# Optimization experiments

Measured on AMD Instinct MI355X. Metric: run time of the kernel, lower is better.

## Reference

```python
import jax, jax.numpy as jnp
import numpy as np
from jax.ops import segment_sum, segment_max

B, P, NP, EP = 128, 16, 256, 1280
EPG, ODIM, NH = 2048, 256, 128
EPS = 1e-5


def _bn(x, g, b):
    # BatchNorm1d (training-mode batch statistics), biased variance like torch
    mu = x.mean(0)
    var = ((x - mu) ** 2).mean(0)
    return g * (x - mu) * jax.lax.rsqrt(var + EPS) + b


def _gat(feat, src, dst, W, al, ar, resW, bias):
    # DGL GATConv: fc -> per-head attn logits -> leaky_relu -> edge softmax over dst -> aggregate; + residual fc + bias
    n = feat.shape[0]
    H, D = al.shape
    z = (feat @ W).reshape(n, H, D)
    el = (z * al).sum(-1)                                  # [n,H]
    er = (z * ar).sum(-1)
    e = jax.nn.leaky_relu(el[src] + er[dst], 0.2)          # [E,H]
    m = segment_max(e, dst, num_segments=n)
    ex = jnp.exp(e - m[dst])
    s = segment_sum(ex, dst, num_segments=n)
    a = ex / (s[dst] + 1e-9)
    rst = segment_sum(a[:, :, None] * z[src], dst, num_segments=n)  # [n,H,D]
    res = (feat @ resW).reshape(n, H, D)
    return (rst + res + bias.reshape(1, H, D)).reshape(n, H * D)


def _plane(feat, src, dst, p):
    # PlaneGraphEncoder forward (eval: dropout off)
    h = _gat(feat, src, dst, p['W1'], p['al1'], p['ar1'], p['res1'], p['b1'])
    h = jax.nn.relu(_bn(h, p['g1'], p['be1']))
    h = _gat(h, src, dst, p['W2'], p['al2'], p['ar2'], p['res2'], p['b2'])
    h = jax.nn.relu(_bn(h, p['g2'], p['be2']))
    rep = h.mean(0)                                        # dgl.mean_nodes -> [32]
    d = jax.nn.relu(_bn(h @ p['dW1'] + p['db1'], p['dg'], p['dbe']))
    recon = d @ p['dW2'] + p['db2']                        # [n,1]
    rloss = jnp.mean((recon - feat) ** 2)
    return rep, rloss


def _masked_gc(h, src, dst, mask_f, W, b):
    # DGL GraphConv(norm='both') with edge_weight = mask[src]*mask[dst]; structural degrees, clamp>=1
    n = h.shape[0]
    ones = jnp.ones(src.shape[0], h.dtype)
    d_out = jnp.maximum(segment_sum(ones, src, num_segments=n), 1.0)
    d_in = jnp.maximum(segment_sum(ones, dst, num_segments=n), 1.0)
    ew = mask_f[src] * mask_f[dst]                         # [E]
    hs = h * jax.lax.rsqrt(d_out)[:, None]
    agg = segment_sum(ew[:, None] * hs[src], dst, num_segments=n)
    return (agg * jax.lax.rsqrt(d_in)[:, None]) @ W + b


def _forward(plane_feat, original_features,
             W1, al1, ar1, res1, b1, g1, be1,
             W2, al2, ar2, res2, b2, g2, be2,
             dW1, db1, dg, dbe, dW2, db2,
             ft_W, ft_b, ft_g, ft_be, gc_W, gc_b, gbn_g, gbn_be,
             c1_W, c1_b, ln_g, ln_be, c2_W, c2_b,
             plane_src, plane_dst, patient_src, patient_dst, mask):
    pp = dict(W1=W1, al1=al1, ar1=ar1, res1=res1, b1=b1, g1=g1, be1=be1,
              W2=W2, al2=al2, ar2=ar2, res2=res2, b2=b2, g2=g2, be2=be2,
              dW1=dW1, db1=db1, dg=dg, dbe=dbe, dW2=dW2, db2=db2)
    enc_b = jax.vmap(_plane, in_axes=(0, 0, 0, None))      # over patients
    enc_pb = jax.vmap(enc_b, in_axes=(1, 1, 1, 0))         # over planes (params axis 0)
    reps, rlosses = enc_pb(plane_feat, plane_src, plane_dst, pp)   # [P,B,32], [P,B]
    plane_rep = jnp.transpose(reps, (1, 0, 2)).reshape(plane_feat.shape[0], -1)  # [B, P*32]
    avg_recon = rlosses.mean()                             # sum / (B*P)

    x = jnp.concatenate([original_features, plane_rep], axis=1)   # [B, fused]
    h = jax.nn.relu(_bn(x @ ft_W + ft_b, ft_g, ft_be))
    mask_f = mask.astype(h.dtype)
    h_sum = h
    for i in range(3):
        hn = _masked_gc(h, patient_src, patient_dst, mask_f, gc_W[i], gc_b[i])
        hn = jax.nn.relu(_bn(hn, gbn_g[i], gbn_be[i]))
        h = hn + h
        h_sum = h_sum + h
    h = h_sum / 4.0                                        # mean over [h0,h1,h2,h3]

    z = h @ c1_W + c1_b
    mu = z.mean(-1, keepdims=True)
    var = ((z - mu) ** 2).mean(-1, keepdims=True)
    z = jax.nn.relu(ln_g * (z - mu) * jax.lax.rsqrt(var + EPS) + ln_be)
    logits = z @ c2_W + c2_b
    return logits, avg_recon


def setup_inputs() -> dict:
    key = jax.random.key(0)
    ks = iter(jax.random.split(key, 64))
    f = lambda shape, s=0.1: jax.random.normal(next(ks), shape, jnp.float32) * s
    inp = dict(
        plane_feat=f((B, P, NP, 1), 1.0),
        plane_src=jax.random.randint(next(ks), (B, P, EP), 0, NP, jnp.int32),
        plane_dst=jax.random.randint(next(ks), (B, P, EP), 0, NP, jnp.int32),
        patient_src=jax.random.randint(next(ks), (EPG,), 0, B, jnp.int32),
        patient_dst=jax.random.randint(next(ks), (EPG,), 0, B, jnp.int32),
        original_features=f((B, ODIM), 1.0),
        mask=jax.random.randint(next(ks), (B,), 0, 2, jnp.int32),
        # per-plane encoder params, stacked over P
        W1=f((P, 1, 128)), al1=f((P, 2, 64)), ar1=f((P, 2, 64)),
        res1=f((P, 1, 128)), b1=f((P, 128)),
        g1=jnp.ones((P, 128)), be1=jnp.zeros((P, 128)),
        W2=f((P, 128, 32)), al2=f((P, 1, 32)), ar2=f((P, 1, 32)),
        res2=f((P, 128, 32)), b2=f((P, 32)),
        g2=jnp.ones((P, 32)), be2=jnp.zeros((P, 32)),
        dW1=f((P, 32, 128)), db1=f((P, 128)),
        dg=jnp.ones((P, 128)), dbe=jnp.zeros((P, 128)),
        dW2=f((P, 128, 1)), db2=f((P, 1)),
        # patient-level params
        ft_W=f((ODIM + P * 32, NH)), ft_b=f((NH,)),
        ft_g=jnp.ones((NH,)), ft_be=jnp.zeros((NH,)),
        gc_W=f((3, NH, NH)), gc_b=f((3, NH)),
        gbn_g=jnp.ones((3, NH)), gbn_be=jnp.zeros((3, NH)),
        c1_W=f((NH, NH // 2)), c1_b=f((NH // 2,)),
        ln_g=jnp.ones((NH // 2,)), ln_be=jnp.zeros((NH // 2,)),
        c2_W=f((NH // 2, 2)), c2_b=f((2,)),
    )
    return inp


def reference(plane_feat, plane_src, plane_dst, patient_src, patient_dst,
              original_features, mask,
              W1, al1, ar1, res1, b1, g1, be1,
              W2, al2, ar2, res2, b2, g2, be2,
              dW1, db1, dg, dbe, dW2, db2,
              ft_W, ft_b, ft_g, ft_be, gc_W, gc_b, gbn_g, gbn_be,
              c1_W, c1_b, ln_g, ln_be, c2_W, c2_b):
    return _forward(plane_feat, original_features,
                    W1, al1, ar1, res1, b1, g1, be1,
                    W2, al2, ar2, res2, b2, g2, be2,
                    dW1, db1, dg, dbe, dW2, db2,
                    ft_W, ft_b, ft_g, ft_be, gc_W, gc_b, gbn_g, gbn_be,
                    c1_W, c1_b, ln_g, ln_be, c2_W, c2_b,
                    plane_src, plane_dst, patient_src, patient_dst, mask)
```

## Files before the change

kernel.cpp:

```cpp
#include <hip/hip_runtime.h>

#define B_    128
#define P_    16
#define NP_   256
#define EP_   1280
#define EPG_  2048
#define ODIM_ 256
#define NH_   128

typedef __attribute__((ext_vector_type(8))) short s8_t;
typedef __attribute__((ext_vector_type(4))) short s4_t;
typedef __attribute__((ext_vector_type(4))) float f4_t;

__device__ __forceinline__ unsigned short f2b(float x) {
  unsigned u = __builtin_bit_cast(unsigned, x);
  u = (u + 0x7fffu + ((u >> 16) & 1u)) >> 16;
  return (unsigned short)u;
}
__device__ __forceinline__ float b2f(short x) {
  unsigned u = ((unsigned)(unsigned short)x) << 16;
  return __builtin_bit_cast(float, u);
}

struct SmemA {
  float f[256];
  union {
    __align__(16) unsigned short wT1[64 * 136];
    __align__(16) unsigned short z2[256 * 40];
  } u1;
  __align__(16) unsigned short dW1T[128 * 36];
  union {
    struct { float S0a[256]; float S1a[256]; } a;
    float redf[512];
  } u2;
  float el2[256], er2[256];
  union {
    struct { float abg0[128], abg1[128], abg2[128]; } a;
    struct { float al2v[32], ar2v[32], dW2v[128]; } b;
  } u3;
  union {
    int cnt[256];
    struct { float scA[32], shA[32], dscA[64], dshA[64]; } b;
  } u4;
  unsigned short esrc[1280];
  int wtot[4];
  float r8[4][8]; float stat[8]; float wA[2], wB[2];
  float rlacc;
};

__global__ __launch_bounds__(256, 3) void plane_enc(
    const float* __restrict__ feat, const int* __restrict__ esrcg, const int* __restrict__ edstg,
    const float* __restrict__ W1, const float* __restrict__ al1, const float* __restrict__ ar1,
    const float* __restrict__ res1, const float* __restrict__ b1, const float* __restrict__ g1,
    const float* __restrict__ be1,
    const float* __restrict__ W2, const float* __restrict__ al2, const float* __restrict__ ar2,
    const float* __restrict__ res2, const float* __restrict__ g2, const float* __restrict__ be2,
    const float* __restrict__ dW1, const float* __restrict__ dg, const float* __restrict__ dbe,
    const float* __restrict__ dW2, const float* __restrict__ db2,
    float* __restrict__ rep_out, float* __restrict__ rloss_out)
{
  __shared__ SmemA s;
  const int g = blockIdx.x;
  const int p = g & 15;
  const int t = threadIdx.x;
  const int lane = t & 63, wv = t >> 6;
  const int l15 = lane & 15, quad = lane >> 4;

  s.f[t] = feat[g * NP_ + t];
  if (t == 0) s.rlacc = 0.f;
  s.u4.cnt[t] = 0;
  __syncthreads();

  const int* gs = esrcg + g * EP_;
  const int* gd = edstg + g * EP_;
  for (int k = t; k < EP_; k += 256) atomicAdd(&s.u4.cnt[gd[k]], 1);
  __syncthreads();
  int v = s.u4.cnt[t];
  int incl = v;
  #pragma unroll
  for (int off = 1; off < 64; off <<= 1) {
    int n = __shfl_up(incl, off, 64);
    if (lane >= off) incl += n;
  }
  if (lane == 63) s.wtot[wv] = incl;
  __syncthreads();
  int woff = 0;
  for (int w = 0; w < wv; w++) woff += s.wtot[w];
  const int myStart = woff + incl - v;
  const int myDeg = v;
  __syncthreads();
  s.u4.cnt[t] = myStart;
  __syncthreads();
  for (int k = t; k < EP_; k += 256) {
    int d = gd[k];
    int pos = atomicAdd(&s.u4.cnt[d], 1);
    s.esrc[pos] = (unsigned short)gs[k];
  }
  {
    const float* W2g = W2 + p * 4096;
    const float* Rg  = res2 + p * 4096;
    for (int q = 0; q < 16; q++) {
      int idx = t + 256 * q;
      int k = idx >> 5, n = idx & 31;
      s.u1.wT1[n * 136 + k]        = f2b(W2g[idx]);
      s.u1.wT1[(n + 32) * 136 + k] = f2b(Rg[idx]);
    }
  }
  if (t < 128) {
    float w1v = W1[p * 128 + t];
    s.el2[t] = w1v * al1[p * 128 + t];
    s.er2[t] = w1v * ar1[p * 128 + t];
  }
  __syncthreads();
  if (t < 2) {
    float a = 0.f, bq = 0.f;
    for (int d2 = 0; d2 < 64; d2++) { a += s.el2[t * 64 + d2]; bq += s.er2[t * 64 + d2]; }
    s.wA[t] = a; s.wB[t] = bq;
  }
  __syncthreads();

  const float fi = s.f[t];
  float S0, S1;
  {
    const float wa0 = s.wA[0], wb0 = s.wB[0], wa1 = s.wA[1], wb1 = s.wB[1];
    float m0 = -1e30f, m1 = -1e30f;
    for (int j = 0; j < myDeg; j++) {
      float fs = s.f[s.esrc[myStart + j]];
      float e0 = wa0 * fs + wb0 * fi; e0 = e0 > 0.f ? e0 : 0.2f * e0;
      float e1 = wa1 * fs + wb1 * fi; e1 = e1 > 0.f ? e1 : 0.2f * e1;
      m0 = fmaxf(m0, e0); m1 = fmaxf(m1, e1);
    }
    float ss0 = 0.f, ss1 = 0.f, U0 = 0.f, U1 = 0.f;
    for (int j = 0; j < myDeg; j++) {
      float fs = s.f[s.esrc[myStart + j]];
      float e0 = wa0 * fs + wb0 * fi; e0 = e0 > 0.f ? e0 : 0.2f * e0;
      float e1 = wa1 * fs + wb1 * fi; e1 = e1 > 0.f ? e1 : 0.2f * e1;
      float x0 = __expf(e0 - m0), x1 = __expf(e1 - m1);
      ss0 += x0; U0 += x0 * fs;
      ss1 += x1; U1 += x1 * fs;
    }
    S0 = U0 / (ss0 + 1e-9f);
    S1 = U1 / (ss1 + 1e-9f);
    s.u2.a.S0a[t] = S0; s.u2.a.S1a[t] = S1;
  }

  {
    float vals[8] = {fi, fi * fi, S0, S0 * S0, S0 * fi, S1, S1 * S1, S1 * fi};
    #pragma unroll
    for (int d2 = 32; d2 > 0; d2 >>= 1) {
      #pragma unroll
      for (int q = 0; q < 8; q++) vals[q] += __shfl_down(vals[q], d2, 64);
    }
    if (lane == 0) {
      #pragma unroll
      for (int q = 0; q < 8; q++) s.r8[wv][q] = vals[q];
    }
  }
  __syncthreads();
  if (t < 8) s.stat[t] = (s.r8[0][t] + s.r8[1][t] + s.r8[2][t] + s.r8[3][t]) * (1.f / 256.f);
  __syncthreads();
  if (t < 128) {
    float mf = s.stat[0], ef2 = s.stat[1];
    int hh = t >> 6;
    float mS = s.stat[2 + 3 * hh], eS2 = s.stat[3 + 3 * hh], eSf = s.stat[4 + 3 * hh];
    float varS = eS2 - mS * mS, varf = ef2 - mf * mf, cov = eSf - mS * mf;
    float Wv = W1[p * 128 + t], Rv = res1[p * 128 + t], Bv = b1[p * 128 + t];
    float mu  = Wv * mS + Rv * mf + Bv;
    float var = Wv * Wv * varS + Rv * Rv * varf + 2.f * Wv * Rv * cov;
    float gn  = g1[p * 128 + t] * rsqrtf(var + 1e-5f);
    s.u3.a.abg0[t] = gn * Wv;
    s.u3.a.abg1[t] = gn * Rv;
    s.u3.a.abg2[t] = gn * (Bv - mu) + be1[p * 128 + t];
  }
  __syncthreads();

  float resv[32];
  {
    f4_t accum[4][4];
    #pragma unroll
    for (int i = 0; i < 4; i++)
      #pragma unroll
      for (int nt = 0; nt < 4; nt++) accum[i][nt] = (f4_t){0.f, 0.f, 0.f, 0.f};

    float fm[4], s0m[4], s1m[4];
    #pragma unroll
    for (int i = 0; i < 4; i++) {
      int m = (wv * 4 + i) * 16 + l15;
      fm[i] = s.f[m]; s0m[i] = s.u2.a.S0a[m]; s1m[i] = s.u2.a.S1a[m];
    }
    #pragma unroll
    for (int kt = 0; kt < 4; kt++) {
      int cbase = kt * 32 + quad * 8;
      float a0[8], a1[8], a2[8];
      #pragma unroll
      for (int j = 0; j < 8; j++) {
        a0[j] = s.u3.a.abg0[cbase + j]; a1[j] = s.u3.a.abg1[cbase + j]; a2[j] = s.u3.a.abg2[cbase + j];
      }
      s8_t afr[4];
      #pragma unroll
      for (int i = 0; i < 4; i++) {
        float Sm = (kt < 2) ? s0m[i] : s1m[i];
        union { s8_t v; unsigned short u[8]; } fu;
        #pragma unroll
        for (int j = 0; j < 8; j++) {
          float h = fmaxf(fmaf(a0[j], Sm, fmaf(a1[j], fm[i], a2[j])), 0.f);
          fu.u[j] = f2b(h);
        }
        afr[i] = fu.v;
      }
      s8_t bfr[4];
      #pragma unroll
      for (int nt = 0; nt < 4; nt++)
        bfr[nt] = *(const s8_t*)&s.u1.wT1[(nt * 16 + l15) * 136 + cbase];
      #pragma unroll
      for (int i = 0; i < 4; i++)
        #pragma unroll
        for (int nt = 0; nt < 4; nt++)
          accum[i][nt] = __builtin_amdgcn_mfma_f32_16x16x32_bf16(afr[i], bfr[nt], accum[i][nt], 0, 0, 0);
    }
    __syncthreads();
    #pragma unroll
    for (int i = 0; i < 4; i++) {
      int mBase = (wv * 4 + i) * 16 + quad * 4;
      #pragma unroll
      for (int nt = 0; nt < 2; nt++) {
        int col = nt * 16 + l15;
        #pragma unroll
        for (int r = 0; r < 4; r++)
          s.u1.z2[(mBase + r) * 40 + col] = f2b(accum[i][nt][r]);
      }
      #pragma unroll
      for (int h2 = 0; h2 < 2; h2++)
        #pragma unroll
        for (int r = 0; r < 4; r++)
          resv[(i * 2 + h2) * 4 + r] = accum[i][2 + h2][r];
    }
  }
  if (t < 32) { s.u3.b.al2v[t] = al2[p * 32 + t]; s.u3.b.ar2v[t] = ar2[p * 32 + t]; }
  if (t < 128) s.u3.b.dW2v[t] = dW2[p * 128 + t];
  {
    const float* Dg = dW1 + p * 4096;
    #pragma unroll
    for (int q = 0; q < 16; q++) {
      int idx = t + 256 * q;
      int k = idx >> 7, n = idx & 127;
      s.dW1T[n * 36 + k] = f2b(Dg[idx]);
    }
  }
  const float db2v = db2[p];
  __syncthreads();

  {
    const s8_t* zr = (const s8_t*)&s.u1.z2[t * 40];
    float el = 0.f, er = 0.f;
    #pragma unroll
    for (int q = 0; q < 4; q++) {
      s8_t vz = zr[q];
      #pragma unroll
      for (int j = 0; j < 8; j++) {
        float zv = b2f(vz[j]);
        el += zv * s.u3.b.al2v[q * 8 + j];
        er += zv * s.u3.b.ar2v[q * 8 + j];
      }
    }
    s.el2[t] = el; s.er2[t] = er;
  }
  __syncthreads();

  float hrow[32];
  {
    const float eri = s.er2[t];
    float m = -1e30f;
    for (int j = 0; j < myDeg; j++) {
      float e = s.el2[s.esrc[myStart + j]] + eri;
      e = e > 0.f ? e : 0.2f * e;
      m = fmaxf(m, e);
    }
    float ss = 0.f;
    #pragma unroll
    for (int d2 = 0; d2 < 32; d2++) hrow[d2] = 0.f;
    for (int j = 0; j < myDeg; j++) {
      int sj = s.esrc[myStart + j];
      float e = s.el2[sj] + eri;
      e = e > 0.f ? e : 0.2f * e;
      float x = __expf(e - m);
      ss += x;
      const s8_t* zr = (const s8_t*)&s.u1.z2[sj * 40];
      #pragma unroll
      for (int q = 0; q < 4; q++) {
        s8_t vz = zr[q];
        #pragma unroll
        for (int jj = 0; jj < 8; jj++) hrow[q * 8 + jj] += x * b2f(vz[jj]);
      }
    }
    float inv = 1.f / (ss + 1e-9f);
    #pragma unroll
    for (int d2 = 0; d2 < 32; d2++) hrow[d2] *= inv;
  }
  __syncthreads();
  #pragma unroll
  for (int i = 0; i < 4; i++) {
    int mBase = (wv * 4 + i) * 16 + quad * 4;
    #pragma unroll
    for (int h2 = 0; h2 < 2; h2++) {
      int col = h2 * 16 + l15;
      #pragma unroll
      for (int r = 0; r < 4; r++)
        s.u1.z2[(mBase + r) * 40 + col] = f2b(resv[(i * 2 + h2) * 4 + r]);
    }
  }
  __syncthreads();
  {
    const s8_t* zr = (const s8_t*)&s.u1.z2[t * 40];
    #pragma unroll
    for (int q = 0; q < 4; q++) {
      s8_t vz = zr[q];
      #pragma unroll
      for (int jj = 0; jj < 8; jj++) hrow[q * 8 + jj] += b2f(vz[jj]);
    }
  }
  #pragma unroll
  for (int d2 = 0; d2 < 32; d2++) s.u1.z2[t * 40 + d2] = f2b(hrow[d2]);
  __syncthreads();

  {
    int c = t & 31, gq = t >> 5;
    float s1 = 0.f, s2 = 0.f;
    for (int j = 0; j < 32; j++) {
      float vz = b2f((short)s.u1.z2[(gq * 32 + j) * 40 + c]);
      s1 += vz; s2 += vz * vz;
    }
    s.u2.redf[t] = s1; s.u2.redf[256 + t] = s2;
  }
  __syncthreads();
  if (t < 32) {
    float s1 = 0.f, s2 = 0.f;
    #pragma unroll
    for (int q = 0; q < 8; q++) { s1 += s.u2.redf[q * 32 + t]; s2 += s.u2.redf[256 + q * 32 + t]; }
    float mu = s1 * (1.f / 256.f);
    float var = s2 * (1.f / 256.f) - mu * mu;
    float a = g2[p * 32 + t] * rsqrtf(var + 1e-5f);
    s.u4.b.scA[t] = a; s.u4.b.shA[t] = be2[p * 32 + t] - a * mu;
  }
  __syncthreads();
  {
    int c = t & 31, gq = t >> 5;
    float a = s.u4.b.scA[c], bb = s.u4.b.shA[c];
    float s1 = 0.f;
    for (int j = 0; j < 32; j++) {
      int ad = (gq * 32 + j) * 40 + c;
      float vz = b2f((short)s.u1.z2[ad]);
      float hv = fmaxf(a * vz + bb, 0.f);
      s.u1.z2[ad] = f2b(hv);
      s1 += hv;
    }
    s.u2.redf[t] = s1;
  }
  __syncthreads();
  if (t < 32) {
    float s1 = 0.f;
    #pragma unroll
    for (int q = 0; q < 8; q++) s1 += s.u2.redf[q * 32 + t];
    rep_out[g * 32 + t] = s1 * (1.f / 256.f);
  }
  __syncthreads();

  {
    s8_t afr2[4];
    #pragma unroll
    for (int i = 0; i < 4; i++)
      afr2[i] = *(const s8_t*)&s.u1.z2[((wv * 4 + i) * 16 + l15) * 40 + quad * 8];
    float rAcc[4][4];
    #pragma unroll
    for (int i = 0; i < 4; i++)
      #pragma unroll
      for (int r = 0; r < 4; r++) rAcc[i][r] = 0.f;

    for (int half = 0; half < 2; half++) {
      __syncthreads();
      s.u2.redf[t] = 0.f; s.u2.redf[256 + t] = 0.f;
      __syncthreads();
      f4_t acc2[4][4];
      #pragma unroll
      for (int i = 0; i < 4; i++)
        #pragma unroll
        for (int nt = 0; nt < 4; nt++) acc2[i][nt] = (f4_t){0.f, 0.f, 0.f, 0.f};
      s8_t bfr[4];
      #pragma unroll
      for (int nt = 0; nt < 4; nt++) {
        const s4_t* pr = (const s4_t*)&s.dW1T[(half * 64 + nt * 16 + l15) * 36 + quad * 8];
        s4_t lo = pr[0], hi = pr[1];
        bfr[nt] = __builtin_shufflevector(lo, hi, 0, 1, 2, 3, 4, 5, 6, 7);
      }
      #pragma unroll
      for (int i = 0; i < 4; i++)
        #pragma unroll
        for (int nt = 0; nt < 4; nt++)
          acc2[i][nt] = __builtin_amdgcn_mfma_f32_16x16x32_bf16(afr2[i], bfr[nt], acc2[i][nt], 0, 0, 0);
      #pragma unroll
      for (int nt = 0; nt < 4; nt++) {
        float s1 = 0.f, s2 = 0.f;
        #pragma unroll
        for (int i = 0; i < 4; i++)
          #pragma unroll
          for (int r = 0; r < 4; r++) { float vv = acc2[i][nt][r]; s1 += vv; s2 += vv * vv; }
        atomicAdd(&s.u2.redf[nt * 16 + l15], s1);
        atomicAdd(&s.u2.redf[256 + nt * 16 + l15], s2);
      }
      __syncthreads();
      if (t < 64) {
        int col = half * 64 + t;
        float mu = s.u2.redf[t] * (1.f / 256.f);
        float var = s.u2.redf[256 + t] * (1.f / 256.f) - mu * mu;
        float a = dg[p * 128 + col] * rsqrtf(var + 1e-5f);
        s.u4.b.dscA[t] = a; s.u4.b.dshA[t] = dbe[p * 128 + col] - a * mu;
      }
      __syncthreads();
      #pragma unroll
      for (int nt = 0; nt < 4; nt++) {
        int cl = nt * 16 + l15;
        float a = s.u4.b.dscA[cl], bb = s.u4.b.dshA[cl], w2 = s.u3.b.dW2v[half * 64 + cl];
        #pragma unroll
        for (int i = 0; i < 4; i++)
          #pragma unroll
          for (int r = 0; r < 4; r++) {
            float dv = fmaxf(a * acc2[i][nt][r] + bb, 0.f);
            rAcc[i][r] += dv * w2;
          }
      }
    }
    #pragma unroll
    for (int off = 1; off < 16; off <<= 1)
      #pragma unroll
      for (int i = 0; i < 4; i++)
        #pragma unroll
        for (int r = 0; r < 4; r++) rAcc[i][r] += __shfl_xor(rAcc[i][r], off, 64);
    if (l15 == 0) {
      float sq = 0.f;
      #pragma unroll
      for (int i = 0; i < 4; i++)
        #pragma unroll
        for (int r = 0; r < 4; r++) {
          int m = (wv * 4 + i) * 16 + quad * 4 + r;
          float diff = rAcc[i][r] + db2v - s.f[m];
          sq += diff * diff;
        }
      atomicAdd(&s.rlacc, sq);
    }
  }
  __syncthreads();
  if (t == 0) atomicAdd(rloss_out, s.rlacc * (1.f / (256.f * 2048.f)));
}

struct SmemB {
  __align__(16) unsigned short arow[128 * 136];
  __align__(16) unsigned short hT[128 * 136];
  union {
    float aB[128 * 132];
    struct {
      union {
        __align__(16) unsigned short wT[128 * 136];
        float zF[128 * 68];
      } w;
      __align__(16) unsigned short aggB[128 * 136];
    } mm;
  } u;
  float redA[1024], redB[1024];
  float facs[128], facd[128], scB[128], shB[128];
  int co[128], ci[128];
};

__global__ __launch_bounds__(1024) void k_patient(
    const float* __restrict__ orig, const float* __restrict__ rep,
    const float* __restrict__ ftW, const float* __restrict__ ftg, const float* __restrict__ ftbe,
    const int* __restrict__ ps, const int* __restrict__ pd, const int* __restrict__ mask,
    const float* __restrict__ gcW, const float* __restrict__ gbng, const float* __restrict__ gbnbe,
    const float* __restrict__ c1W, const float* __restrict__ c1b,
    const float* __restrict__ lng, const float* __restrict__ lnbe,
    const float* __restrict__ c2W, const float* __restrict__ c2b,
    const float* __restrict__ rl, float* __restrict__ out)
{
  __shared__ SmemB s;
  const int t = threadIdx.x;
  const int w = t >> 6, lane = t & 63;
  const int l15 = lane & 15, quad = lane >> 4;
  const int mb = w & 7, nb = (w >> 3) * 64;

  if (t < 128) { s.co[t] = 0; s.ci[t] = 0; }
  for (int idx = t; idx < 128 * 132; idx += 1024) s.u.aB[idx] = 0.f;
  __syncthreads();
  for (int e = t; e < EPG_; e += 1024) { atomicAdd(&s.co[ps[e]], 1); atomicAdd(&s.ci[pd[e]], 1); }
  __syncthreads();
  if (t < 128) {
    float mk = (float)mask[t];
    int da = s.co[t] > 1 ? s.co[t] : 1;
    int db = s.ci[t] > 1 ? s.ci[t] : 1;
    s.facs[t] = mk * rsqrtf((float)da);
    s.facd[t] = mk * rsqrtf((float)db);
  }
  for (int e = t; e < EPG_; e += 1024) atomicAdd(&s.u.aB[pd[e] * 132 + ps[e]], 1.f);
  __syncthreads();
  for (int idx = t; idx < 16384; idx += 1024) {
    int d = idx >> 7, sN = idx & 127;
    s.arow[d * 136 + sN] = f2b(s.u.aB[d * 132 + sN] * s.facd[d] * s.facs[sN]);
  }
  __syncthreads();

  f4_t acc[4];
  #pragma unroll
  for (int nt = 0; nt < 4; nt++) acc[nt] = (f4_t){0.f, 0.f, 0.f, 0.f};
  const int m = mb * 16 + l15;
  for (int chunk = 0; chunk < 6; chunk++) {
    #pragma unroll
    for (int q = 0; q < 16; q++) {
      int idx = t + 1024 * q;
      int kk = idx >> 7, n = idx & 127;
      s.u.mm.w.wT[n * 136 + kk] = f2b(ftW[(chunk * 128 + kk) * 128 + n]);
    }
    __syncthreads();
    #pragma unroll
    for (int ks = 0; ks < 4; ks++) {
      int k0 = chunk * 128 + ks * 32 + quad * 8;
      const float* px = (k0 < 256) ? (orig + m * 256 + k0) : (rep + m * 512 + (k0 - 256));
      float4 xa = ((const float4*)px)[0];
      float4 xb = ((const float4*)px)[1];
      union { s8_t v; unsigned short u[8]; } fu;
      fu.u[0] = f2b(xa.x); fu.u[1] = f2b(xa.y); fu.u[2] = f2b(xa.z); fu.u[3] = f2b(xa.w);
      fu.u[4] = f2b(xb.x); fu.u[5] = f2b(xb.y); fu.u[6] = f2b(xb.z); fu.u[7] = f2b(xb.w);
      #pragma unroll
      for (int nt = 0; nt < 4; nt++) {
        s8_t bfr = *(const s8_t*)&s.u.mm.w.wT[(nb + nt * 16 + l15) * 136 + ks * 32 + quad * 8];
        acc[nt] = __builtin_amdgcn_mfma_f32_16x16x32_bf16(fu.v, bfr, acc[nt], 0, 0, 0);
      }
    }
    __syncthreads();
  }

  float hR[16], hsumR[16];
  {
    #pragma unroll
    for (int nt = 0; nt < 4; nt++) {
      float s1 = acc[nt][0] + acc[nt][1] + acc[nt][2] + acc[nt][3];
      float s2 = acc[nt][0]*acc[nt][0] + acc[nt][1]*acc[nt][1] + acc[nt][2]*acc[nt][2] + acc[nt][3]*acc[nt][3];
      s1 += __shfl_xor(s1, 16, 64); s1 += __shfl_xor(s1, 32, 64);
      s2 += __shfl_xor(s2, 16, 64); s2 += __shfl_xor(s2, 32, 64);
      if (quad == 0) {
        s.redA[mb * 128 + nb + nt * 16 + l15] = s1;
        s.redB[mb * 128 + nb + nt * 16 + l15] = s2;
      }
    }
    __syncthreads();
    if (t < 128) {
      float a1 = 0.f, a2 = 0.f;
      #pragma unroll
      for (int q = 0; q < 8; q++) { a1 += s.redA[q * 128 + t]; a2 += s.redB[q * 128 + t]; }
      float mu = a1 * (1.f / 128.f), var = a2 * (1.f / 128.f) - mu * mu;
      float a = ftg[t] * rsqrtf(var + 1e-5f);
      s.scB[t] = a; s.shB[t] = ftbe[t] - a * mu;
    }
    __syncthreads();
    #pragma unroll
    for (int nt = 0; nt < 4; nt++) {
      int col = nb + nt * 16 + l15;
      float a = s.scB[col], bb = s.shB[col];
      #pragma unroll
      for (int r = 0; r < 4; r++) {
        int row = mb * 16 + quad * 4 + r;
        float hv = fmaxf(a * acc[nt][r] + bb, 0.f);
        hR[nt * 4 + r] = hv; hsumR[nt * 4 + r] = hv;
        s.hT[col * 136 + row] = f2b(hv);
      }
    }
  }
  __syncthreads();

  for (int layer = 0; layer < 3; layer++) {
    #pragma unroll
    for (int q = 0; q < 16; q++) {
      int idx = t + 1024 * q;
      int kk = idx >> 7, n = idx & 127;
      s.u.mm.w.wT[n * 136 + kk] = f2b(gcW[layer * 16384 + kk * 128 + n]);
    }
    f4_t ag[4];
    #pragma unroll
    for (int nt = 0; nt < 4; nt++) ag[nt] = (f4_t){0.f, 0.f, 0.f, 0.f};
    #pragma unroll
    for (int ks = 0; ks < 4; ks++) {
      s8_t afr = *(const s8_t*)&s.arow[(mb * 16 + l15) * 136 + ks * 32 + quad * 8];
      #pragma unroll
      for (int nt = 0; nt < 4; nt++) {
        s8_t bfr = *(const s8_t*)&s.hT[(nb + nt * 16 + l15) * 136 + ks * 32 + quad * 8];
        ag[nt] = __builtin_amdgcn_mfma_f32_16x16x32_bf16(afr, bfr, ag[nt], 0, 0, 0);
      }
    }
    #pragma unroll
    for (int nt = 0; nt < 4; nt++) {
      int col = nb + nt * 16 + l15;
      #pragma unroll
      for (int r = 0; r < 4; r++)
        s.u.mm.aggB[(mb * 16 + quad * 4 + r) * 136 + col] = f2b(ag[nt][r]);
    }
    __syncthreads();
    f4_t oc[4];
    #pragma unroll
    for (int nt = 0; nt < 4; nt++) oc[nt] = (f4_t){0.f, 0.f, 0.f, 0.f};
    #pragma unroll
    for (int ks = 0; ks < 4; ks++) {
      s8_t afr = *(const s8_t*)&s.u.mm.aggB[(mb * 16 + l15) * 136 + ks * 32 + quad * 8];
      #pragma unroll
      for (int nt = 0; nt < 4; nt++) {
        s8_t bfr = *(const s8_t*)&s.u.mm.w.wT[(nb + nt * 16 + l15) * 136 + ks * 32 + quad * 8];
        oc[nt] = __builtin_amdgcn_mfma_f32_16x16x32_bf16(afr, bfr, oc[nt], 0, 0, 0);
      }
    }
    #pragma unroll
    for (int nt = 0; nt < 4; nt++) {
      float s1 = oc[nt][0] + oc[nt][1] + oc[nt][2] + oc[nt][3];
      float s2 = oc[nt][0]*oc[nt][0] + oc[nt][1]*oc[nt][1] + oc[nt][2]*oc[nt][2] + oc[nt][3]*oc[nt][3];
      s1 += __shfl_xor(s1, 16, 64); s1 += __shfl_xor(s1, 32, 64);
      s2 += __shfl_xor(s2, 16, 64); s2 += __shfl_xor(s2, 32, 64);
      if (quad == 0) {
        s.redA[mb * 128 + nb + nt * 16 + l15] = s1;
        s.redB[mb * 128 + nb + nt * 16 + l15] = s2;
      }
    }
    __syncthreads();
    if (t < 128) {
      float a1 = 0.f, a2 = 0.f;
      #pragma unroll
      for (int q = 0; q < 8; q++) { a1 += s.redA[q * 128 + t]; a2 += s.redB[q * 128 + t]; }
      float mu = a1 * (1.f / 128.f), var = a2 * (1.f / 128.f) - mu * mu;
      float a = gbng[layer * 128 + t] * rsqrtf(var + 1e-5f);
      s.scB[t] = a; s.shB[t] = gbnbe[layer * 128 + t] - a * mu;
    }
    __syncthreads();
    #pragma unroll
    for (int nt = 0; nt < 4; nt++) {
      int col = nb + nt * 16 + l15;
      float a = s.scB[col], bb = s.shB[col];
      #pragma unroll
      for (int r = 0; r < 4; r++) {
        int row = mb * 16 + quad * 4 + r;
        float hn = fmaxf(a * oc[nt][r] + bb, 0.f) + hR[nt * 4 + r];
        hR[nt * 4 + r] = hn;
        hsumR[nt * 4 + r] += hn;
        s.hT[col * 136 + row] = f2b(hn);
      }
    }
    __syncthreads();
  }

  #pragma unroll
  for (int nt = 0; nt < 4; nt++) {
    int col = nb + nt * 16 + l15;
    #pragma unroll
    for (int r = 0; r < 4; r++)
      s.u.mm.aggB[(mb * 16 + quad * 4 + r) * 136 + col] = f2b(hsumR[nt * 4 + r] * 0.25f);
  }
  #pragma unroll
  for (int q = 0; q < 8; q++) {
    int idx = t + 1024 * q;
    int n = idx & 63, kk = idx >> 6;
    s.u.mm.w.wT[n * 136 + kk] = f2b(c1W[kk * 64 + n]);
  }
  __syncthreads();
  {
    const int nb2 = (w >> 3) * 32;
    f4_t zc[2];
    #pragma unroll
    for (int nt = 0; nt < 2; nt++) zc[nt] = (f4_t){0.f, 0.f, 0.f, 0.f};
    #pragma unroll
    for (int ks = 0; ks < 4; ks++) {
      s8_t afr = *(const s8_t*)&s.u.mm.aggB[(mb * 16 + l15) * 136 + ks * 32 + quad * 8];
      #pragma unroll
      for (int nt = 0; nt < 2; nt++) {
        s8_t bfr = *(const s8_t*)&s.u.mm.w.wT[(nb2 + nt * 16 + l15) * 136 + ks * 32 + quad * 8];
        zc[nt] = __builtin_amdgcn_mfma_f32_16x16x32_bf16(afr, bfr, zc[nt], 0, 0, 0);
      }
    }
    __syncthreads();
    #pragma unroll
    for (int nt = 0; nt < 2; nt++) {
      int col = nb2 + nt * 16 + l15;
      #pragma unroll
      for (int r = 0; r < 4; r++)
        s.u.mm.w.zF[(mb * 16 + quad * 4 + r) * 68 + col] = zc[nt][r] + c1b[col];
    }
  }
  __syncthreads();
  if (t < 128) {
    float s1 = 0.f, s2 = 0.f;
    #pragma unroll
    for (int j = 0; j < 64; j++) { float zv = s.u.mm.w.zF[t * 68 + j]; s1 += zv; s2 += zv * zv; }
    float mu = s1 * (1.f / 64.f);
    float var = s2 * (1.f / 64.f) - mu * mu;
    float rs = rsqrtf(var + 1e-5f);
    float l0 = 0.f, l1 = 0.f;
    #pragma unroll
    for (int j = 0; j < 64; j++) {
      float zv = s.u.mm.w.zF[t * 68 + j];
      float zn = fmaxf(lng[j] * (zv - mu) * rs + lnbe[j], 0.f);
      l0 += zn * c2W[j * 2];
      l1 += zn * c2W[j * 2 + 1];
    }
    out[t * 2]     = l0 + c2b[0];
    out[t * 2 + 1] = l1 + c2b[1];
  }
  if (t == 0) out[256] = rl[0];
}

extern "C" void kernel_launch(void* const* d_in, const int* in_sizes, int n_in,
                              void* d_out, int out_size, void* d_ws, size_t ws_size,
                              hipStream_t stream) {
  (void)in_sizes; (void)n_in; (void)out_size; (void)ws_size;
  const float* plane_feat  = (const float*)d_in[0];
  const int*   plane_src   = (const int*)d_in[1];
  const int*   plane_dst   = (const int*)d_in[2];
  const int*   patient_src = (const int*)d_in[3];
  const int*   patient_dst = (const int*)d_in[4];
  const float* orig        = (const float*)d_in[5];
  const int*   mask        = (const int*)d_in[6];
  const float* W1   = (const float*)d_in[7];
  const float* al1  = (const float*)d_in[8];
  const float* ar1  = (const float*)d_in[9];
  const float* res1 = (const float*)d_in[10];
  const float* b1   = (const float*)d_in[11];
  const float* g1   = (const float*)d_in[12];
  const float* be1  = (const float*)d_in[13];
  const float* W2   = (const float*)d_in[14];
  const float* al2  = (const float*)d_in[15];
  const float* ar2  = (const float*)d_in[16];
  const float* res2 = (const float*)d_in[17];
  const float* g2   = (const float*)d_in[19];
  const float* be2  = (const float*)d_in[20];
  const float* dW1  = (const float*)d_in[21];
  const float* dg   = (const float*)d_in[23];
  const float* dbe  = (const float*)d_in[24];
  const float* dW2  = (const float*)d_in[25];
  const float* db2  = (const float*)d_in[26];
  const float* ftW  = (const float*)d_in[27];
  const float* ftg  = (const float*)d_in[29];
  const float* ftbe = (const float*)d_in[30];
  const float* gcW  = (const float*)d_in[31];
  const float* gbng = (const float*)d_in[33];
  const float* gbnbe= (const float*)d_in[34];
  const float* c1W  = (const float*)d_in[35];
  const float* c1b  = (const float*)d_in[36];
  const float* lng  = (const float*)d_in[37];
  const float* lnbe = (const float*)d_in[38];
  const float* c2W  = (const float*)d_in[39];
  const float* c2b  = (const float*)d_in[40];

  float* ws   = (float*)d_ws;
  float* rep  = ws;
  float* rl   = ws + 131328;
  float* outp = (float*)d_out;

  hipMemsetAsync(rl, 0, sizeof(float), stream);
  plane_enc<<<2048, 256, 0, stream>>>(plane_feat, plane_src, plane_dst,
      W1, al1, ar1, res1, b1, g1, be1, W2, al2, ar2, res2, g2, be2,
      dW1, dg, dbe, dW2, db2, rep, rl);
  k_patient<<<1, 1024, 0, stream>>>(orig, rep, ftW, ftg, ftbe,
      patient_src, patient_dst, mask,
      gcW, gbng, gbnbe, c1W, c1b, lng, lnbe, c2W, c2b, rl, outp);
}
```

Before: 352.4 us.

## Split patient feature-transform matmul and adjacency build into separate multi-block kernel

```diff
diff --git a/kernel.cpp b/kernel.cpp
--- a/kernel.cpp
+++ b/kernel.cpp
@@ -57,7 +57,7 @@
     const float* __restrict__ res2, const float* __restrict__ g2, const float* __restrict__ be2,
     const float* __restrict__ dW1, const float* __restrict__ dg, const float* __restrict__ dbe,
     const float* __restrict__ dW2, const float* __restrict__ db2,
-    float* __restrict__ rep_out, float* __restrict__ rloss_out)
+    float* __restrict__ rep_out, float* __restrict__ rlp_out)
 {
   __shared__ SmemA s;
   const int g = blockIdx.x;
@@ -449,14 +449,83 @@
     }
   }
   __syncthreads();
-  if (t == 0) atomicAdd(rloss_out, s.rlacc * (1.f / (256.f * 2048.f)));
+  if (t == 0) rlp_out[g] = s.rlacc;
+}
+
+__global__ __launch_bounds__(256) void ft_mm(
+    const float* __restrict__ orig, const float* __restrict__ rep,
+    const float* __restrict__ ftW, float* __restrict__ hpre,
+    const int* __restrict__ ps, const int* __restrict__ pd,
+    const int* __restrict__ mask, unsigned short* __restrict__ abar)
+{
+  const int t = threadIdx.x;
+
+  if (blockIdx.x == 8) {
+    __shared__ int aB[128 * 128];
+    __shared__ int co[128], ci[128];
+    __shared__ float facs[128], facd[128];
+    for (int idx = t; idx < 16384; idx += 256) aB[idx] = 0;
+    if (t < 128) { co[t] = 0; ci[t] = 0; }
+    __syncthreads();
+    for (int e = t; e < EPG_; e += 256) {
+      int sN = ps[e], d = pd[e];
+      atomicAdd(&co[sN], 1);
+      atomicAdd(&ci[d], 1);
+      atomicAdd(&aB[d * 128 + sN], 1);
+    }
+    __syncthreads();
+    if (t < 128) {
+      float mk = (float)mask[t];
+      int da = co[t] > 1 ? co[t] : 1;
+      int db = ci[t] > 1 ? ci[t] : 1;
+      facs[t] = mk * rsqrtf((float)da);
+      facd[t] = mk * rsqrtf((float)db);
+    }
+    __syncthreads();
+    for (int idx = t; idx < 16384; idx += 256) {
+      int d = idx >> 7, sN = idx & 127;
+      abar[idx] = f2b((float)aB[idx] * facd[d] * facs[sN]);
+    }
+    return;
+  }
+
+  const int wv = t >> 6, lane = t & 63;
+  const int l15 = lane & 15, quad = lane >> 4;
+  const int m = blockIdx.x * 16 + l15;
+
+  f4_t acc[2];
+  acc[0] = (f4_t){0.f, 0.f, 0.f, 0.f};
+  acc[1] = (f4_t){0.f, 0.f, 0.f, 0.f};
+  for (int kt = 0; kt < 24; kt++) {
+    int k0 = kt * 32 + quad * 8;
+    const float* px = (k0 < 256) ? (orig + m * 256 + k0) : (rep + m * 512 + (k0 - 256));
+    float4 xa = ((const float4*)px)[0];
+    float4 xb = ((const float4*)px)[1];
+    union { s8_t v; unsigned short u[8]; } fu;
+    fu.u[0] = f2b(xa.x); fu.u[1] = f2b(xa.y); fu.u[2] = f2b(xa.z); fu.u[3] = f2b(xa.w);
+    fu.u[4] = f2b(xb.x); fu.u[5] = f2b(xb.y); fu.u[6] = f2b(xb.z); fu.u[7] = f2b(xb.w);
+    #pragma unroll
+    for (int nt = 0; nt < 2; nt++) {
+      int col = wv * 32 + nt * 16 + l15;
+      union { s8_t v; unsigned short u[8]; } bu;
+      #pragma unroll
+      for (int j = 0; j < 8; j++) bu.u[j] = f2b(ftW[(k0 + j) * 128 + col]);
+      acc[nt] = __builtin_amdgcn_mfma_f32_16x16x32_bf16(fu.v, bu.v, acc[nt], 0, 0, 0);
+    }
+  }
+  #pragma unroll
+  for (int nt = 0; nt < 2; nt++) {
+    int col = wv * 32 + nt * 16 + l15;
+    #pragma unroll
+    for (int r = 0; r < 4; r++)
+      hpre[(blockIdx.x * 16 + quad * 4 + r) * 128 + col] = acc[nt][r];
+  }
 }
 
 struct SmemB {
   __align__(16) unsigned short arow[128 * 136];
   __align__(16) unsigned short hT[128 * 136];
   union {
-    float aB[128 * 132];
     struct {
       union {
         __align__(16) unsigned short wT[128 * 136];
@@ -466,19 +535,17 @@
     } mm;
   } u;
   float redA[1024], redB[1024];
-  float facs[128], facd[128], scB[128], shB[128];
-  int co[128], ci[128];
+  float scB[128], shB[128];
 };
 
 __global__ __launch_bounds__(1024) void k_patient(
-    const float* __restrict__ orig, const float* __restrict__ rep,
-    const float* __restrict__ ftW, const float* __restrict__ ftg, const float* __restrict__ ftbe,
-    const int* __restrict__ ps, const int* __restrict__ pd, const int* __restrict__ mask,
+    const float* __restrict__ hpre, const unsigned short* __restrict__ abar,
+    const float* __restrict__ ftg, const float* __restrict__ ftbe,
     const float* __restrict__ gcW, const float* __restrict__ gbng, const float* __restrict__ gbnbe,
     const float* __restrict__ c1W, const float* __restrict__ c1b,
     const float* __restrict__ lng, const float* __restrict__ lnbe,
     const float* __restrict__ c2W, const float* __restrict__ c2b,
-    const float* __restrict__ rl, float* __restrict__ out)
+    const float* __restrict__ rlp, float* __restrict__ out)
 {
   __shared__ SmemB s;
   const int t = threadIdx.x;
@@ -486,54 +553,18 @@
   const int l15 = lane & 15, quad = lane >> 4;
   const int mb = w & 7, nb = (w >> 3) * 64;
 
-  if (t < 128) { s.co[t] = 0; s.ci[t] = 0; }
-  for (int idx = t; idx < 128 * 132; idx += 1024) s.u.aB[idx] = 0.f;
-  __syncthreads();
-  for (int e = t; e < EPG_; e += 1024) { atomicAdd(&s.co[ps[e]], 1); atomicAdd(&s.ci[pd[e]], 1); }
-  __syncthreads();
-  if (t < 128) {
-    float mk = (float)mask[t];
-    int da = s.co[t] > 1 ? s.co[t] : 1;
-    int db = s.ci[t] > 1 ? s.ci[t] : 1;
-    s.facs[t] = mk * rsqrtf((float)da);
-    s.facd[t] = mk * rsqrtf((float)db);
-  }
-  for (int e = t; e < EPG_; e += 1024) atomicAdd(&s.u.aB[pd[e] * 132 + ps[e]], 1.f);
-  __syncthreads();
   for (int idx = t; idx < 16384; idx += 1024) {
     int d = idx >> 7, sN = idx & 127;
-    s.arow[d * 136 + sN] = f2b(s.u.aB[d * 132 + sN] * s.facd[d] * s.facs[sN]);
-  }
-  __syncthreads();
+    s.arow[d * 136 + sN] = abar[idx];
+  }
 
   f4_t acc[4];
   #pragma unroll
-  for (int nt = 0; nt < 4; nt++) acc[nt] = (f4_t){0.f, 0.f, 0.f, 0.f};
-  const int m = mb * 16 + l15;
-  for (int chunk = 0; chunk < 6; chunk++) {
-    #pragma unroll
-    for (int q = 0; q < 16; q++) {
-      int idx = t + 1024 * q;
-      int kk = idx >> 7, n = idx & 127;
-      s.u.mm.w.wT[n * 136 + kk] = f2b(ftW[(chunk * 128 + kk) * 128 + n]);
-    }
-    __syncthreads();
-    #pragma unroll
-    for (int ks = 0; ks < 4; ks++) {
-      int k0 = chunk * 128 + ks * 32 + quad * 8;
-      const float* px = (k0 < 256) ? (orig + m * 256 + k0) : (rep + m * 512 + (k0 - 256));
-      float4 xa = ((const float4*)px)[0];
-      float4 xb = ((const float4*)px)[1];
-      union { s8_t v; unsigned short u[8]; } fu;
-      fu.u[0] = f2b(xa.x); fu.u[1] = f2b(xa.y); fu.u[2] = f2b(xa.z); fu.u[3] = f2b(xa.w);
-      fu.u[4] = f2b(xb.x); fu.u[5] = f2b(xb.y); fu.u[6] = f2b(xb.z); fu.u[7] = f2b(xb.w);
-      #pragma unroll
-      for (int nt = 0; nt < 4; nt++) {
-        s8_t bfr = *(const s8_t*)&s.u.mm.w.wT[(nb + nt * 16 + l15) * 136 + ks * 32 + quad * 8];
-        acc[nt] = __builtin_amdgcn_mfma_f32_16x16x32_bf16(fu.v, bfr, acc[nt], 0, 0, 0);
-      }
-    }
-    __syncthreads();
+  for (int nt = 0; nt < 4; nt++) {
+    int col = nb + nt * 16 + l15;
+    #pragma unroll
+    for (int r = 0; r < 4; r++)
+      acc[nt][r] = hpre[(mb * 16 + quad * 4 + r) * 128 + col];
   }
 
   float hR[16], hsumR[16];
@@ -706,7 +737,20 @@
     out[t * 2]     = l0 + c2b[0];
     out[t * 2 + 1] = l1 + c2b[1];
   }
-  if (t == 0) out[256] = rl[0];
+
+  {
+    float r = rlp[t] + rlp[t + 1024];
+    #pragma unroll
+    for (int off = 32; off > 0; off >>= 1) r += __shfl_down(r, off, 64);
+    if (lane == 0) s.redA[w] = r;
+  }
+  __syncthreads();
+  if (t == 0) {
+    float tot = 0.f;
+    #pragma unroll
+    for (int i = 0; i < 16; i++) tot += s.redA[i];
+    out[256] = tot * (1.f / (256.f * 2048.f));
+  }
 }
 
 extern "C" void kernel_launch(void* const* d_in, const int* in_sizes, int n_in,
@@ -753,14 +797,16 @@
 
   float* ws   = (float*)d_ws;
   float* rep  = ws;
-  float* rl   = ws + 131328;
+  float* hpre = ws + 65536;
+  unsigned short* abar = (unsigned short*)(ws + 81920);
+  float* rlp  = ws + 90112;
   float* outp = (float*)d_out;
 
-  hipMemsetAsync(rl, 0, sizeof(float), stream);
   plane_enc<<<2048, 256, 0, stream>>>(plane_feat, plane_src, plane_dst,
       W1, al1, ar1, res1, b1, g1, be1, W2, al2, ar2, res2, g2, be2,
-      dW1, dg, dbe, dW2, db2, rep, rl);
-  k_patient<<<1, 1024, 0, stream>>>(orig, rep, ftW, ftg, ftbe,
-      patient_src, patient_dst, mask,
-      gcW, gbng, gbnbe, c1W, c1b, lng, lnbe, c2W, c2b, rl, outp);
+      dW1, dg, dbe, dW2, db2, rep, rlp);
+  ft_mm<<<9, 256, 0, stream>>>(orig, rep, ftW, hpre,
+      patient_src, patient_dst, mask, abar);
+  k_patient<<<1, 1024, 0, stream>>>(hpre, abar, ftg, ftbe,
+      gcW, gbng, gbnbe, c1W, c1b, lng, lnbe, c2W, c2b, rlp, outp);
 }
```

Measured after the change: 318.9 us. 1.1x faster.
